# Performance work log

Measured on AMD Instinct MI355X. Metric: run time of the kernel, lower is better.

Reference implementation:

```python
import jax, jax.numpy as jnp
import numpy as np

EPS = 1e-5

def layer_norm(x, gamma, beta):
    # biased variance (unbiased=False), matching torch code
    mean = jnp.mean(x, axis=-1, keepdims=True)
    var = jnp.mean((x - mean) ** 2, axis=-1, keepdims=True)
    return (x - mean) / jnp.sqrt(var + EPS) * gamma + beta

def setup_inputs() -> dict:
    key = jax.random.key(0)
    ks = jax.random.split(key, 8)
    B, T, C, H = 2, 2048, 768, 12
    Dff = 4 * C
    s = lambda n: 1.0 / np.sqrt(n)
    return {
        "x": jax.random.normal(ks[0], (B, T, C), dtype=jnp.float32),
        "mask": jnp.ones((B, T), dtype=jnp.int32),
        "Wqkv": jax.random.normal(ks[1], (C, 3 * C), dtype=jnp.float32) * s(C),
        "bqkv": jnp.zeros((3 * C,), dtype=jnp.float32),
        "Wp": jax.random.normal(ks[2], (C, C), dtype=jnp.float32) * s(C),
        "bp": jnp.zeros((C,), dtype=jnp.float32),
        "gamma1": jnp.ones((1, 1, C), dtype=jnp.float32),
        "beta1": jnp.zeros((1, 1, C), dtype=jnp.float32),
        "W1": jax.random.normal(ks[3], (C, Dff), dtype=jnp.float32) * s(C),
        "b1": jnp.zeros((Dff,), dtype=jnp.float32),
        "W2": jax.random.normal(ks[4], (Dff, C), dtype=jnp.float32) * s(Dff),
        "b2": jnp.zeros((C,), dtype=jnp.float32),
        "gamma2": jnp.ones((1, 1, C), dtype=jnp.float32),
        "beta2": jnp.zeros((1, 1, C), dtype=jnp.float32),
    }

def reference(x, mask, Wqkv, bqkv, Wp, bp, gamma1, beta1, W1, b1, W2, b2, gamma2, beta2):
    B, T, C = x.shape
    H = 12
    D = C // H
    # --- multi-head attention (hand-rolled QK^T-softmax-V) ---
    qkv = x @ Wqkv + bqkv                                  # (B,T,3C)
    q, k, v = jnp.split(qkv, 3, axis=-1)
    q = q.reshape(B, T, H, D).transpose(0, 2, 1, 3)        # (B,H,T,D)
    k = k.reshape(B, T, H, D).transpose(0, 2, 1, 3)
    v = v.reshape(B, T, H, D).transpose(0, 2, 1, 3)
    scores = jnp.einsum('bhtd,bhsd->bhts', q, k) * (D ** -0.5)  # (B,H,T,T)
    pad = (mask == 0)[:, None, None, :]                    # (B,1,1,T)
    scores = jnp.where(pad, -jnp.inf, scores)
    weights = jax.nn.softmax(scores, axis=-1)
    attn = jnp.einsum('bhts,bhsd->bhtd', weights, v)       # (B,H,T,D)
    attn = attn.transpose(0, 2, 1, 3).reshape(B, T, C)
    attn = attn @ Wp + bp
    # --- post-sublayer LN then residual (as in source) ---
    out = x + layer_norm(attn, gamma1, beta1)
    # --- MLP with exact GELU ---
    h = jax.nn.gelu(out @ W1 + b1, approximate=False)
    mlp = h @ W2 + b2
    out = out + layer_norm(mlp, gamma2, beta2)
    return out
```

## Files before the change

### kernel.cpp

```cpp
#include <hip/hip_runtime.h>
#include <math.h>

#define BB 2
#define TT 2048
#define CC 768
#define NH 12
#define HD 64
#define DFF 3072
#define MM (BB*TT)

typedef _Float16 f16;
typedef unsigned long long u64;
typedef unsigned int u32;
typedef __attribute__((ext_vector_type(8))) _Float16 f16x8;
typedef __attribute__((ext_vector_type(4))) _Float16 f16x4;
typedef __attribute__((ext_vector_type(4))) float f32x4;
typedef __attribute__((ext_vector_type(2))) unsigned int u32x2;
typedef __attribute__((ext_vector_type(4))) unsigned int u32x4;

#define QSCALE 0.18033688011112042f

#define GLD_LDS(gptr, lptr) \
  __builtin_amdgcn_global_load_lds((const __attribute__((address_space(1))) void*)(gptr), \
                                   (__attribute__((address_space(3))) void*)(lptr), 16, 0, 0)

#if __has_builtin(__builtin_amdgcn_exp2f)
#define EXP2(x) __builtin_amdgcn_exp2f(x)
#else
#define EXP2(x) exp2f(x)
#endif

#if __has_builtin(__builtin_amdgcn_rcpf)
#define RCP(x) __builtin_amdgcn_rcpf(x)
#else
#define RCP(x) (1.f / (x))
#endif

#if __has_builtin(__builtin_amdgcn_permlane32_swap) && __has_builtin(__builtin_amdgcn_permlane16_swap)
#define HAVE_PERMLANE_SWAP 1
#else
#define HAVE_PERMLANE_SWAP 0
#endif

__device__ __forceinline__ u32 pkrtz(float a, float b)
{
    auto h = __builtin_amdgcn_cvt_pkrtz(a, b);
    return __builtin_bit_cast(u32, h);
}

__device__ __forceinline__ float gelu_f(float x)
{
    const float y = fabsf(x) * 0.70710678118654752f;
    const float t = RCP(fmaf(0.3275911f, y, 1.f));
    float p = fmaf(1.061405429f, t, -1.453152027f);
    p = fmaf(p, t, 1.421413741f);
    p = fmaf(p, t, -0.284496736f);
    p = fmaf(p, t, 0.254829592f);
    p = p * t;
    const float e = EXP2(-y * y * 1.4426950408889634f);
    const float er = copysignf(1.f - p * e, x);
    return 0.5f * x * (1.f + er);
}

__device__ __forceinline__ void transpose_tile(const float* __restrict__ W,
                                               f16* __restrict__ Wt,
                                               int K, int N, int idx,
                                               float tile[32][33])
{
    const int kx = idx % (K / 32), ny = idx / (K / 32);
    const int k0 = kx * 32, n0 = ny * 32;
    const int r  = threadIdx.x >> 3;
    const int c4 = (threadIdx.x & 7) * 4;
    float4 v = *(const float4*)&W[(size_t)(k0 + r) * N + n0 + c4];
    tile[r][c4 + 0] = v.x; tile[r][c4 + 1] = v.y;
    tile[r][c4 + 2] = v.z; tile[r][c4 + 3] = v.w;
    __syncthreads();
    f16x4 o = {(f16)tile[c4 + 0][r], (f16)tile[c4 + 1][r],
               (f16)tile[c4 + 2][r], (f16)tile[c4 + 3][r]};
    *(f16x4*)&Wt[(size_t)(n0 + r) * K + k0 + c4] = o;
}

__global__ __launch_bounds__(256)
void conv_all(const float* __restrict__ x, f16* __restrict__ xh,
              const float* __restrict__ Wqkv, f16* __restrict__ Wqkvt,
              const float* __restrict__ Wp, f16* __restrict__ Wpt,
              const float* __restrict__ W1, f16* __restrict__ W1t,
              const float* __restrict__ W2, f16* __restrict__ W2t)
{
    __shared__ float tile[32][33];
    const int blk = blockIdx.x;
    if (blk < 3072) {
        const int i = blk * 256 + threadIdx.x;
        float4 v = ((const float4*)x)[i];
        f16x4 o = {(f16)v.x, (f16)v.y, (f16)v.z, (f16)v.w};
        ((f16x4*)xh)[i] = o;
    } else if (blk < 4800) {
        transpose_tile(Wqkv, Wqkvt, CC, 3 * CC, blk - 3072, tile);
    } else if (blk < 5376) {
        transpose_tile(Wp, Wpt, CC, CC, blk - 4800, tile);
    } else if (blk < 7680) {
        transpose_tile(W1, W1t, CC, DFF, blk - 5376, tile);
    } else {
        transpose_tile(W2, W2t, DFF, CC, blk - 7680, tile);
    }
}

template<int TM, int OUT_MODE, int GELU, int SPLITK, int AMODE>
__global__ __launch_bounds__(256)
void gemm_mfma(const f16* __restrict__ A, const f16* __restrict__ Bt,
               const float* __restrict__ bias, void* __restrict__ Cout,
               f16* __restrict__ Kout, f16* __restrict__ Vout,
               const int* __restrict__ maskp, int M, int N, int K,
               const f16* __restrict__ Ao1,
               const float* __restrict__ lp0, const float* __restrict__ lp1)
{
    constexpr int NT = (TM == 128) ? 4 : 2;
    constexpr int G  = 512 / TM;
    __shared__ f16 As[2][TM * 32];
    __shared__ f16 Bs[2][128 * 32];

    int id = blockIdx.x;
    int kk = 0;
    if (SPLITK == 2) { kk = id & 1; id >>= 1; }
    const int xcd = id & 7, j = id >> 3;
    const int by = xcd * G + (j & (G - 1));
    const int bx = j / G;
    const int Keff = K / SPLITK;

    const int t = threadIdx.x;
    const int lane = t & 63, w = t >> 6;
    const int fr = lane & 15, quad = lane >> 4;
    const int row0 = by * TM, col0 = bx * 128;
    const int wm = (TM == 128) ? (w & 1) * 64 : 0;
    const int wn = (TM == 128) ? (w >> 1) * 64 : w * 32;

    const int arow = w * (TM / 4) + (lane >> 2);
    const int brow = w * 32 + (lane >> 2);
    const int cg = (((lane & 3) ^ ((lane >> 3) & 3)) * 16);
    const char* ag = (const char*)(A  + (size_t)(row0 + arow) * K + kk * Keff) + cg;
    const char* bg = (const char*)(Bt + (size_t)(col0 + brow) * K + kk * Keff) + cg;
    const size_t rowK = (size_t)K * 2;
    const int wA = w * (TM / 4) * 32;
    const int wB = w * 32 * 32;
    const int sof = (quad ^ ((fr >> 1) & 3)) * 8;

    const f16 *a0p = nullptr, *a1p = nullptr;
    const float *lr0 = nullptr, *lr1 = nullptr;
    int lchunk8 = 0;
    f16* aswb[2] = {nullptr, nullptr};
    if (AMODE) {
        const int strow = lane >> 2, pchunk = lane & 3;
        lchunk8 = ((pchunk ^ ((lane >> 3) & 3))) * 8;
        const int ar = row0 + w * 16 + strow;
        a0p = A   + (size_t)ar * K + kk * Keff + lchunk8;
        a1p = Ao1 + (size_t)ar * K + kk * Keff + lchunk8;
        lr0 = lp0 + ar * NH;
        lr1 = lp1 + ar * NH;
        aswb[0] = &As[0][wA + strow * 32 + pchunk * 8];
        aswb[1] = &As[1][wA + strow * 32 + pchunk * 8];
    }

    f32x4 acc[4][NT] = {};

    if (AMODE) {
        f16x8 a0 = *(const f16x8*)(a0p);
        f16x8 a1 = *(const f16x8*)(a1p);
        const int hh = (kk * Keff + lchunk8) >> 6;
        const f16 lh = (f16)RCP(lr0[hh] + lr1[hh]);
        f16x8 s;
#pragma unroll
        for (int jj = 0; jj < 8; ++jj) s[jj] = (f16)((a0[jj] + a1[jj]) * lh);
        *(f16x8*)aswb[0] = s;
    } else {
        GLD_LDS(ag, &As[0][wA]);
        if (TM == 128) GLD_LDS(ag + 16 * rowK, &As[0][wA + 16 * 32]);
    }
    GLD_LDS(bg, &Bs[0][wB]);
    GLD_LDS(bg + 16 * rowK, &Bs[0][wB + 16 * 32]);

    for (int k0 = 0; k0 < Keff; k0 += 32) {
        const int buf = (k0 >> 5) & 1;
        f16x8 na0, na1; float nls = 1.f;
        if (AMODE && k0 + 32 < Keff) {
            na0 = *(const f16x8*)(a0p + k0 + 32);
            na1 = *(const f16x8*)(a1p + k0 + 32);
            const int hh = (kk * Keff + k0 + 32 + lchunk8) >> 6;
            nls = lr0[hh] + lr1[hh];
        }
        __syncthreads();
        if (k0 + 32 < Keff) {
            const size_t kb = (size_t)(k0 + 32) * 2;
            if (AMODE) {
                const f16 lh = (f16)RCP(nls);
                f16x8 s;
#pragma unroll
                for (int jj = 0; jj < 8; ++jj) s[jj] = (f16)((na0[jj] + na1[jj]) * lh);
                *(f16x8*)aswb[buf ^ 1] = s;
            } else {
                GLD_LDS(ag + kb, &As[buf ^ 1][wA]);
                if (TM == 128) GLD_LDS(ag + kb + 16 * rowK, &As[buf ^ 1][wA + 16 * 32]);
            }
            GLD_LDS(bg + kb, &Bs[buf ^ 1][wB]);
            GLD_LDS(bg + kb + 16 * rowK, &Bs[buf ^ 1][wB + 16 * 32]);
        }
        f16x8 af[4], bf[NT];
#pragma unroll
        for (int mt = 0; mt < 4; ++mt)
            af[mt] = *(const f16x8*)&As[buf][(wm + mt * 16 + fr) * 32 + sof];
#pragma unroll
        for (int nt = 0; nt < NT; ++nt)
            bf[nt] = *(const f16x8*)&Bs[buf][(wn + nt * 16 + fr) * 32 + sof];
#pragma unroll
        for (int mt = 0; mt < 4; ++mt)
#pragma unroll
            for (int nt = 0; nt < NT; ++nt)
                acc[mt][nt] = __builtin_amdgcn_mfma_f32_16x16x32_f16(
                    af[mt], bf[nt], acc[mt][nt], 0, 0, 0);
    }

    float bvs[NT];
#pragma unroll
    for (int nt = 0; nt < NT; ++nt)
        bvs[nt] = (SPLITK == 2 && kk) ? 0.f : bias[col0 + wn + nt * 16 + fr];
    f16* outbase = (f16*)Cout + (SPLITK == 2 ? (size_t)kk * M * N : 0);
#pragma unroll
    for (int mt = 0; mt < 4; ++mt) {
        const int rowb = row0 + wm + mt * 16 + quad * 4;
        float mv[4] = {1.f, 1.f, 1.f, 1.f};
        if (OUT_MODE == 2 && col0 >= 1536) {
            int4 mi = *(const int4*)&maskp[rowb];
            mv[0] = mi.x ? 1.f : 0.f; mv[1] = mi.y ? 1.f : 0.f;
            mv[2] = mi.z ? 1.f : 0.f; mv[3] = mi.w ? 1.f : 0.f;
        }
#pragma unroll
        for (int nt = 0; nt < NT; ++nt) {
            const int col = col0 + wn + nt * 16 + fr;
            if (OUT_MODE == 2) {
                const int bq = rowb >> 11, sb = rowb & 2047;
                if (col0 < 768) {
#pragma unroll
                    for (int v = 0; v < 4; ++v)
                        ((f16*)Cout)[(size_t)(rowb + v) * 768 + col]
                            = (f16)((acc[mt][nt][v] + bvs[nt]) * QSCALE);
                } else if (col0 < 1536) {
                    const int dg = col - 768;
                    const int hh = dg >> 6, dd = dg & 63;
                    f16* kb = Kout + (size_t)(bq * NH + hh) * (TT * HD);
#pragma unroll
                    for (int v = 0; v < 4; ++v) {
                        const int s = sb + v;
                        kb[((s >> 4) * 128 + (dd >> 3) * 16 + (s & 15)) * 8 + (dd & 7)]
                            = (f16)(acc[mt][nt][v] + bvs[nt]);
                    }
                } else {
                    const int dg = col - 1536;
                    const int hh = dg >> 6, dd = dg & 63;
                    f16* vb = Vout + (size_t)(bq * NH + hh) * (TT * HD);
                    f16x4 pk = {(f16)((acc[mt][nt][0] + bvs[nt]) * mv[0]),
                                (f16)((acc[mt][nt][1] + bvs[nt]) * mv[1]),
                                (f16)((acc[mt][nt][2] + bvs[nt]) * mv[2]),
                                (f16)((acc[mt][nt][3] + bvs[nt]) * mv[3])};
                    *(f16x4*)&vb[((sb >> 3) * 64 + dd) * 8 + (sb & 7)] = pk;
                }
            } else {
#pragma unroll
                for (int v = 0; v < 4; ++v) {
                    float o = acc[mt][nt][v] + bvs[nt];
                    if (GELU) o = gelu_f(o);
                    outbase[(size_t)(rowb + v) * N + col] = (f16)o;
                }
            }
        }
    }
}

__global__ __launch_bounds__(256, 3)
void attn_mfma(const f16* __restrict__ qh, const f16* __restrict__ kth,
               const f16* __restrict__ vth, const int* __restrict__ mask,
               f16* __restrict__ O0, f16* __restrict__ O1,
               float* __restrict__ l0, float* __restrict__ l1)
{
    __shared__ __align__(16) char smem[16640];
    f16* Mf = (f16*)smem;
#if !HAVE_PERMLANE_SWAP
    f16* Ps = (f16*)(smem + 4096);
#endif
    float* Ored  = (float*)smem;
    float* lredp = (float*)(smem + 16384);

    const int id = blockIdx.x;
    const int xcd = id & 7, j = id >> 3;
    const int pair = xcd * 3 + j % 3;
    const int rem = j / 3;
    const int qt = rem >> 1, shalf = rem & 1;
    const int b = pair / NH, h = pair % NH;

    const int t = threadIdx.x, lane = t & 63, w = t >> 6;
    const int wq = w >> 1, ws = w & 1;
    const int fr = lane & 15, quad = lane >> 4;

    {
        int4 mi0 = *(const int4*)&mask[b * TT + t * 8];
        int4 mi1 = *(const int4*)&mask[b * TT + t * 8 + 4];
        f16x8 mrow;
        mrow[0] = mi0.x ? (f16)1.f : (f16)0.f; mrow[1] = mi0.y ? (f16)1.f : (f16)0.f;
        mrow[2] = mi0.z ? (f16)1.f : (f16)0.f; mrow[3] = mi0.w ? (f16)1.f : (f16)0.f;
        mrow[4] = mi1.x ? (f16)1.f : (f16)0.f; mrow[5] = mi1.y ? (f16)1.f : (f16)0.f;
        mrow[6] = mi1.z ? (f16)1.f : (f16)0.f; mrow[7] = mi1.w ? (f16)1.f : (f16)0.f;
        *(f16x8*)&Mf[t * 8] = mrow;
    }

    f16x8 qf[2][2];
#pragma unroll
    for (int nt = 0; nt < 2; ++nt)
#pragma unroll
        for (int ks = 0; ks < 2; ++ks)
            qf[nt][ks] = *(const f16x8*)&qh[(size_t)(b * TT + qt * 64 + wq * 32 + nt * 16 + fr) * CC
                                            + h * HD + ks * 32 + quad * 8];

    __syncthreads();

    const f16* KB = kth + (size_t)(b * NH + h) * (TT * HD);
    const f16* VB = vth + (size_t)(b * NH + h) * (TT * HD);
    int ko[2][2], vo[4];
#pragma unroll
    for (int mt = 0; mt < 2; ++mt)
#pragma unroll
        for (int ks = 0; ks < 2; ++ks)
            ko[mt][ks] = ((ws * 2 + mt) * 128 + (ks * 4 + quad) * 16 + fr) * 8;
#pragma unroll
    for (int nt = 0; nt < 4; ++nt)
        vo[nt] = ((ws * 4 + quad) * 64 + nt * 16 + fr) * 8;

    f32x4 oacc[2][4] = {};
    f32x4 lacc[2] = {};

    const int it0 = shalf * 16;
#pragma unroll 2
    for (int it = it0; it < it0 + 16; ++it) {
        const int ib = it * 4096;
        f16x8 vf[4];
#pragma unroll
        for (int nt = 0; nt < 4; ++nt)
            vf[nt] = *(const f16x8*)(VB + ib + vo[nt]);
        f16x8 kf[2][2];
#pragma unroll
        for (int mt = 0; mt < 2; ++mt)
#pragma unroll
            for (int ks = 0; ks < 2; ++ks)
                kf[mt][ks] = *(const f16x8*)(KB + ib + ko[mt][ks]);

        f32x4 sacc[2][2] = {};
#pragma unroll
        for (int mt = 0; mt < 2; ++mt)
#pragma unroll
            for (int nt = 0; nt < 2; ++nt) {
                sacc[mt][nt] = __builtin_amdgcn_mfma_f32_16x16x32_f16(
                    kf[mt][0], qf[nt][0], sacc[mt][nt], 0, 0, 0);
                sacc[mt][nt] = __builtin_amdgcn_mfma_f32_16x16x32_f16(
                    kf[mt][1], qf[nt][1], sacc[mt][nt], 0, 0, 0);
            }

        f16x8 mf = *(const f16x8*)&Mf[it * 64 + ws * 32 + quad * 8];

#if HAVE_PERMLANE_SWAP
#pragma unroll
        for (int nt = 0; nt < 2; ++nt) {
            const u32 pa = pkrtz(EXP2(sacc[0][nt][0]), EXP2(sacc[0][nt][1]));
            const u32 pb = pkrtz(EXP2(sacc[0][nt][2]), EXP2(sacc[0][nt][3]));
            const u32 pc = pkrtz(EXP2(sacc[1][nt][0]), EXP2(sacc[1][nt][1]));
            const u32 pd = pkrtz(EXP2(sacc[1][nt][2]), EXP2(sacc[1][nt][3]));
            const u32x2 e0 = __builtin_amdgcn_permlane32_swap(pa, pc, false, false);
            const u32x2 e1 = __builtin_amdgcn_permlane16_swap(e0.x, e0.y, false, false);
            const u32x2 e2 = __builtin_amdgcn_permlane32_swap(pb, pd, false, false);
            const u32x2 e3 = __builtin_amdgcn_permlane16_swap(e2.x, e2.y, false, false);
            const u32x4 pw = {e1.x, e3.x, e1.y, e3.y};
            const f16x8 pfr = __builtin_bit_cast(f16x8, pw);
            lacc[nt] = __builtin_amdgcn_mfma_f32_16x16x32_f16(pfr, mf, lacc[nt], 0, 0, 0);
#pragma unroll
            for (int vt = 0; vt < 4; ++vt)
                oacc[nt][vt] = __builtin_amdgcn_mfma_f32_16x16x32_f16(
                    pfr, vf[vt], oacc[nt][vt], 0, 0, 0);
        }
#else
#pragma unroll
        for (int mt = 0; mt < 2; ++mt)
#pragma unroll
            for (int nt = 0; nt < 2; ++nt) {
                f16x4 pk = {(f16)EXP2(sacc[mt][nt][0]), (f16)EXP2(sacc[mt][nt][1]),
                            (f16)EXP2(sacc[mt][nt][2]), (f16)EXP2(sacc[mt][nt][3])};
                *(f16x4*)&Ps[(wq * 32 + nt * 16 + fr) * 72 + ws * 32 + mt * 16 + quad * 4] = pk;
            }
        f16x8 pf[2];
#pragma unroll
        for (int mt = 0; mt < 2; ++mt)
            pf[mt] = *(const f16x8*)&Ps[(wq * 32 + mt * 16 + fr) * 72 + ws * 32 + quad * 8];
#pragma unroll
        for (int mt = 0; mt < 2; ++mt) {
            lacc[mt] = __builtin_amdgcn_mfma_f32_16x16x32_f16(pf[mt], mf, lacc[mt], 0, 0, 0);
#pragma unroll
            for (int nt = 0; nt < 4; ++nt)
                oacc[mt][nt] = __builtin_amdgcn_mfma_f32_16x16x32_f16(
                    pf[mt], vf[nt], oacc[mt][nt], 0, 0, 0);
        }
#endif
    }

    f16* Oout = shalf ? O1 : O0;
    float* lout = shalf ? l1 : l0;
    __syncthreads();
    if (ws == 1) {
#pragma unroll
        for (int mt = 0; mt < 2; ++mt) {
            const int q = wq * 32 + mt * 16 + quad * 4;
#pragma unroll
            for (int nt = 0; nt < 4; ++nt)
#pragma unroll
                for (int v = 0; v < 4; ++v)
                    Ored[(q + v) * 64 + nt * 16 + fr] = oacc[mt][nt][v];
            if (fr == 0)
#pragma unroll
                for (int v = 0; v < 4; ++v) lredp[q + v] = lacc[mt][v];
        }
    }
    __syncthreads();
    if (ws == 0) {
#pragma unroll
        for (int mt = 0; mt < 2; ++mt) {
            const int q0 = wq * 32 + mt * 16 + quad * 4;
            if (fr == 0)
#pragma unroll
                for (int v = 0; v < 4; ++v)
                    lout[(size_t)(b * TT + qt * 64 + q0 + v) * NH + h]
                        = lacc[mt][v] + lredp[q0 + v];
#pragma unroll
            for (int nt = 0; nt < 4; ++nt)
#pragma unroll
                for (int v = 0; v < 4; ++v) {
                    float o = oacc[mt][nt][v] + Ored[(q0 + v) * 64 + nt * 16 + fr];
                    Oout[(size_t)(b * TT + qt * 64 + q0 + v) * CC + h * HD + nt * 16 + fr]
                        = (f16)o;
                }
        }
    }
}

template<int WRITE_H>
__global__ __launch_bounds__(256)
void ln_residual(const float* __restrict__ res,
                 const f16* __restrict__ y0, const f16* __restrict__ y1,
                 const float* __restrict__ gamma, const float* __restrict__ beta,
                 float* __restrict__ outp, f16* __restrict__ outh)
{
    const int t = threadIdx.x;
    const int row = blockIdx.x * 8 + (t >> 5);
    const int c0 = (t & 31) * 24;
    const f16* yr0 = y0 + (size_t)row * CC + c0;
    const f16* yr1 = y1 + (size_t)row * CC + c0;
    float v[24];
    float s = 0.f, sq = 0.f;
#pragma unroll
    for (int i = 0; i < 3; ++i) {
        f16x8 a = *(const f16x8*)(yr0 + i * 8);
        f16x8 bb = *(const f16x8*)(yr1 + i * 8);
#pragma unroll
        for (int jj = 0; jj < 8; ++jj) {
            float vv = (float)a[jj] + (float)bb[jj];
            v[i * 8 + jj] = vv; s += vv; sq += vv * vv;
        }
    }
#pragma unroll
    for (int off = 1; off < 32; off <<= 1) {
        s  += __shfl_xor(s, off);
        sq += __shfl_xor(sq, off);
    }
    const float mean = s * (1.f / 768.f);
    const float var  = sq * (1.f / 768.f) - mean * mean;
    const float rstd = rsqrtf(var + 1e-5f);
    const float* rr = res + (size_t)row * CC + c0;
    float* orow = outp + (size_t)row * CC + c0;
#pragma unroll
    for (int i = 0; i < 6; ++i) {
        float4 r4 = *(const float4*)(rr + i * 4);
        float4 g4 = *(const float4*)(gamma + c0 + i * 4);
        float4 b4 = *(const float4*)(beta + c0 + i * 4);
        float4 o;
        o.x = r4.x + (v[i*4+0] - mean) * rstd * g4.x + b4.x;
        o.y = r4.y + (v[i*4+1] - mean) * rstd * g4.y + b4.y;
        o.z = r4.z + (v[i*4+2] - mean) * rstd * g4.z + b4.z;
        o.w = r4.w + (v[i*4+3] - mean) * rstd * g4.w + b4.w;
        *(float4*)(orow + i * 4) = o;
        if (WRITE_H) {
            f16x4 h4 = {(f16)o.x, (f16)o.y, (f16)o.z, (f16)o.w};
            *(f16x4*)(outh + (size_t)row * CC + c0 + i * 4) = h4;
        }
    }
}

extern "C" void kernel_launch(void* const* d_in, const int* in_sizes, int n_in,
                              void* d_out, int out_size, void* d_ws, size_t ws_size,
                              hipStream_t stream)
{
    const float* x     = (const float*)d_in[0];
    const int*   mask  = (const int*)  d_in[1];
    const float* Wqkv  = (const float*)d_in[2];
    const float* bqkv  = (const float*)d_in[3];
    const float* Wp    = (const float*)d_in[4];
    const float* bp    = (const float*)d_in[5];
    const float* g1    = (const float*)d_in[6];
    const float* be1   = (const float*)d_in[7];
    const float* W1    = (const float*)d_in[8];
    const float* b1    = (const float*)d_in[9];
    const float* W2    = (const float*)d_in[10];
    const float* b2    = (const float*)d_in[11];
    const float* g2    = (const float*)d_in[12];
    const float* be2   = (const float*)d_in[13];
    float* outp = (float*)d_out;

    char* wsb = (char*)d_ws;
    f16*   qhb    = (f16*)(wsb);
    f16*   kth    = (f16*)(wsb + 6291456);
    f16*   vth    = (f16*)(wsb + 12582912);
    f16*   O0     = (f16*)(wsb + 18874368);
    f16*   O1     = (f16*)(wsb + 25165824);
    f16*   hbuf   = (f16*)(wsb);
    f16*   xh     = (f16*)(wsb + 25165824);
    float* out1f  = (float*)(wsb + 25165824);
    f16*   Wqkvt  = (f16*)(wsb + 31457280);
    f16*   Wpt    = (f16*)(wsb + 34996224);
    f16*   W1t    = (f16*)(wsb + 37748736);
    f16*   W2t    = (f16*)(wsb + 42467328);
    f16*   p0     = (f16*)(wsb + 47185920);
    f16*   p1     = (f16*)(wsb + 53477376);
    f16*   out1h  = (f16*)(wsb + 59768832);
    float* l0     = (float*)(wsb + 66060288);
    float* l1     = (float*)(wsb + 66256896);

    const dim3 blk(256);

    conv_all<<<dim3(9984), blk, 0, stream>>>(x, xh, Wqkv, Wqkvt, Wp, Wpt,
                                             W1, W1t, W2, W2t);

    gemm_mfma<128, 2, 0, 1, 0><<<dim3((3 * CC / 128) * (MM / 128)), blk, 0, stream>>>(
        xh, Wqkvt, bqkv, qhb, kth, vth, mask, MM, 3 * CC, CC,
        nullptr, nullptr, nullptr);
    attn_mfma<<<dim3((TT / 64) * NH * BB * 2), blk, 0, stream>>>(
        qhb, kth, vth, mask, O0, O1, l0, l1);
    gemm_mfma<64, 1, 0, 2, 1><<<dim3(2 * (CC / 128) * (MM / 64)), blk, 0, stream>>>(
        O0, Wpt, bp, p0, nullptr, nullptr, nullptr, MM, CC, CC,
        O1, l0, l1);
    ln_residual<1><<<dim3(MM / 8), blk, 0, stream>>>(x, p0, p1, g1, be1, out1f, out1h);
    gemm_mfma<64, 1, 1, 1, 0><<<dim3((DFF / 128) * (MM / 64)), blk, 0, stream>>>(
        out1h, W1t, b1, hbuf, nullptr, nullptr, nullptr, MM, DFF, CC,
        nullptr, nullptr, nullptr);
    gemm_mfma<64, 1, 0, 2, 0><<<dim3(2 * (CC / 128) * (MM / 64)), blk, 0, stream>>>(
        hbuf, W2t, b2, p0, nullptr, nullptr, nullptr, MM, CC, DFF,
        nullptr, nullptr, nullptr);
    ln_residual<0><<<dim3(MM / 8), blk, 0, stream>>>(out1f, p0, p1, g2, be2, outp, nullptr);
}
```

Before: 280.0 us.

## Pre-tile MLP operands into MFMA fragment layout and load them directly without LDS

Adds a fragment-tiled layout (16-row by 32-k blocks) for W1, W2, the LN1 half-precision output and the GELU hidden buffer. A new GEMM kernel reads MFMA operand fragments straight from global memory, skipping LDS staging and barriers, and replaces both MLP GEMMs. The W2 GEMM also moves to a smaller 32-row tile with split-K. The aim is to remove LDS traffic and synchronisation overhead. In exchange, operand reuse now depends on caches rather than shared memory, and there is no software prefetch.

Result: slower. 290.2 us (+3.6%).

```diff
diff --git a/kernel.cpp b/kernel.cpp
--- a/kernel.cpp
+++ b/kernel.cpp
@@ -46,6 +46,12 @@
 {
     auto h = __builtin_amdgcn_cvt_pkrtz(a, b);
     return __builtin_bit_cast(u32, h);
+}
+
+__device__ __forceinline__ size_t ftile(int r, int k, int K)
+{
+    return ((size_t)(r >> 4) * (K >> 5) + (k >> 5)) * 512
+         + (size_t)(((k >> 3) & 3) * 128 + (r & 15) * 8 + (k & 7));
 }
 
 __device__ __forceinline__ float gelu_f(float x)
@@ -64,7 +70,7 @@
 
 __device__ __forceinline__ void transpose_tile(const float* __restrict__ W,
                                                f16* __restrict__ Wt,
-                                               int K, int N, int idx,
+                                               int K, int N, int idx, int tiled,
                                                float tile[32][33])
 {
     const int kx = idx % (K / 32), ny = idx / (K / 32);
@@ -77,7 +83,10 @@
     __syncthreads();
     f16x4 o = {(f16)tile[c4 + 0][r], (f16)tile[c4 + 1][r],
                (f16)tile[c4 + 2][r], (f16)tile[c4 + 3][r]};
-    *(f16x4*)&Wt[(size_t)(n0 + r) * K + k0 + c4] = o;
+    if (tiled)
+        *(f16x4*)&Wt[ftile(n0 + r, k0 + c4, K)] = o;
+    else
+        *(f16x4*)&Wt[(size_t)(n0 + r) * K + k0 + c4] = o;
 }
 
 __global__ __launch_bounds__(256)
@@ -95,13 +104,92 @@
         f16x4 o = {(f16)v.x, (f16)v.y, (f16)v.z, (f16)v.w};
         ((f16x4*)xh)[i] = o;
     } else if (blk < 4800) {
-        transpose_tile(Wqkv, Wqkvt, CC, 3 * CC, blk - 3072, tile);
+        transpose_tile(Wqkv, Wqkvt, CC, 3 * CC, blk - 3072, 0, tile);
     } else if (blk < 5376) {
-        transpose_tile(Wp, Wpt, CC, CC, blk - 4800, tile);
+        transpose_tile(Wp, Wpt, CC, CC, blk - 4800, 0, tile);
     } else if (blk < 7680) {
-        transpose_tile(W1, W1t, CC, DFF, blk - 5376, tile);
+        transpose_tile(W1, W1t, CC, DFF, blk - 5376, 1, tile);
     } else {
-        transpose_tile(W2, W2t, DFF, CC, blk - 7680, tile);
+        transpose_tile(W2, W2t, DFF, CC, blk - 7680, 1, tile);
+    }
+}
+
+template<int WM, int GELU, int SPLITK, int OUTT>
+__global__ __launch_bounds__(256)
+void gemm_direct(const f16* __restrict__ At, const f16* __restrict__ Btt,
+                 const float* __restrict__ bias, f16* __restrict__ Cout,
+                 int M, int N, int K)
+{
+    constexpr int MT = WM / 16;
+    int id = blockIdx.x;
+    int kk = 0;
+    if (SPLITK == 2) { kk = id & 1; id >>= 1; }
+    const int G = 512 / WM;
+    const int xcd = id & 7, j = id >> 3;
+    const int by = xcd * G + (j & (G - 1));
+    const int bx = j / G;
+    const int Keff = K / SPLITK;
+
+    const int t = threadIdx.x, lane = t & 63, w = t >> 6;
+    const int fr = lane & 15, quad = lane >> 4;
+    const int row0 = by * WM;
+    const int col0 = bx * 128 + w * 32;
+
+    const int KT = K >> 5;
+    const int kt0 = (kk * Keff) >> 5;
+
+    const f16* pA[MT];
+#pragma unroll
+    for (int mt = 0; mt < MT; ++mt)
+        pA[mt] = At + ((size_t)((row0 >> 4) + mt) * KT + kt0) * 512
+                    + quad * 128 + fr * 8;
+    const f16* pB[2];
+#pragma unroll
+    for (int nt = 0; nt < 2; ++nt)
+        pB[nt] = Btt + ((size_t)((col0 >> 4) + nt) * KT + kt0) * 512
+                     + quad * 128 + fr * 8;
+
+    f32x4 acc[MT][2] = {};
+
+#pragma unroll 4
+    for (int ks = 0; ks < Keff / 32; ++ks) {
+        f16x8 af[MT], bf[2];
+#pragma unroll
+        for (int mt = 0; mt < MT; ++mt)
+            af[mt] = *(const f16x8*)(pA[mt] + ks * 512);
+#pragma unroll
+        for (int nt = 0; nt < 2; ++nt)
+            bf[nt] = *(const f16x8*)(pB[nt] + ks * 512);
+#pragma unroll
+        for (int mt = 0; mt < MT; ++mt)
+#pragma unroll
+            for (int nt = 0; nt < 2; ++nt)
+                acc[mt][nt] = __builtin_amdgcn_mfma_f32_16x16x32_f16(
+                    af[mt], bf[nt], acc[mt][nt], 0, 0, 0);
+    }
+
+    float bv[2];
+#pragma unroll
+    for (int nt = 0; nt < 2; ++nt)
+        bv[nt] = (SPLITK == 2 && kk) ? 0.f : bias[col0 + nt * 16 + fr];
+#pragma unroll
+    for (int mt = 0; mt < MT; ++mt) {
+        const int rowb = row0 + mt * 16 + quad * 4;
+#pragma unroll
+        for (int nt = 0; nt < 2; ++nt) {
+            const int col = col0 + nt * 16 + fr;
+#pragma unroll
+            for (int v = 0; v < 4; ++v) {
+                float o = acc[mt][nt][v] + bv[nt];
+                if (GELU) o = gelu_f(o);
+                if (OUTT == 1) {
+                    f16* outb = Cout + (SPLITK == 2 ? (size_t)kk * M * N : 0);
+                    outb[(size_t)(rowb + v) * N + col] = (f16)o;
+                } else {
+                    Cout[ftile(rowb + v, col, N)] = (f16)o;
+                }
+            }
+        }
     }
 }
 
@@ -492,7 +580,7 @@
         *(float4*)(orow + i * 4) = o;
         if (WRITE_H) {
             f16x4 h4 = {(f16)o.x, (f16)o.y, (f16)o.z, (f16)o.w};
-            *(f16x4*)(outh + (size_t)row * CC + c0 + i * 4) = h4;
+            *(f16x4*)&outh[ftile(row, c0 + i * 4, CC)] = h4;
         }
     }
 }
@@ -550,11 +638,9 @@
         O0, Wpt, bp, p0, nullptr, nullptr, nullptr, MM, CC, CC,
         O1, l0, l1);
     ln_residual<1><<<dim3(MM / 8), blk, 0, stream>>>(x, p0, p1, g1, be1, out1f, out1h);
-    gemm_mfma<64, 1, 1, 1, 0><<<dim3((DFF / 128) * (MM / 64)), blk, 0, stream>>>(
-        out1h, W1t, b1, hbuf, nullptr, nullptr, nullptr, MM, DFF, CC,
-        nullptr, nullptr, nullptr);
-    gemm_mfma<64, 1, 0, 2, 0><<<dim3(2 * (CC / 128) * (MM / 64)), blk, 0, stream>>>(
-        hbuf, W2t, b2, p0, nullptr, nullptr, nullptr, MM, CC, DFF,
-        nullptr, nullptr, nullptr);
+    gemm_direct<64, 1, 1, 2><<<dim3((MM / 64) * (DFF / 128)), blk, 0, stream>>>(
+        out1h, W1t, b1, hbuf, MM, DFF, CC);
+    gemm_direct<32, 0, 2, 1><<<dim3(2 * (MM / 32) * (CC / 128)), blk, 0, stream>>>(
+        hbuf, W2t, b2, p0, MM, CC, DFF);
     ln_residual<0><<<dim3(MM / 8), blk, 0, stream>>>(out1f, p0, p1, g2, be2, outp, nullptr);
 }
```
